# Optimization experiments

Hardware: AMD Instinct MI355X
Metric: run time of the kernel (lower is better)

## Reference

```python
import jax, jax.numpy as jnp
import numpy as np

B, H, F, G = 32768, 256, 32, 16
N = F * G * 2  # total number of heads


def setup_inputs() -> dict:
    key = jax.random.key(0)
    kx, kw, kb = jax.random.split(key, 3)
    x = jax.random.normal(kx, (B, H), dtype=jnp.float32)
    # stacked weights/biases of all N = in_features*granularity*2 Linear(H,1) heads
    W = jax.random.normal(kw, (N, H), dtype=jnp.float32) * (1.0 / jnp.sqrt(H))
    b = jax.random.normal(kb, (N,), dtype=jnp.float32) * 0.01
    return {"x": x, "W": W, "b": b}


def reference(x, W, b):
    # Fused equivalent of N independent Linear(H,1)+Sigmoid heads:
    # one [B,H] x [H,N] matmul + bias + sigmoid, then reshape to [B,F,G,2].
    z = jax.nn.sigmoid(jnp.einsum("bh,nh->bn", x, W) + b)
    return z.reshape(x.shape[0], F, G, 2)
```

## Files before the change

### kernel.cpp

```cpp
#include <hip/hip_runtime.h>
#include <hip/hip_fp16.h>

typedef _Float16 half8 __attribute__((ext_vector_type(8)));
typedef _Float16 half4 __attribute__((ext_vector_type(4)));
typedef float floatx4 __attribute__((ext_vector_type(4)));

#define KH 256
#define NN 1024
#define BM 64
#define BN 64
#define LDW 264
#define NT (NN / BN)

__global__ __launch_bounds__(256, 2)
void lfh_kernel(const float* __restrict__ x, const float* __restrict__ W,
                const float* __restrict__ bias, float* __restrict__ out) {
    __shared__ _Float16 Ws[2][BN * LDW];

    const int t   = threadIdx.x;
    const int w   = t >> 6;
    const int l   = t & 63;
    const int l15 = l & 15;
    const int lq  = l >> 4;
    const int m0  = blockIdx.x * BM;

    half8 afrag[8];
    {
        const int arow = m0 + w * 16 + l15;
        const float* xr = x + (size_t)arow * KH;
        #pragma unroll
        for (int ks = 0; ks < 8; ++ks) {
            const int kb = ks * 32 + lq * 8;
            floatx4 lo = *(const floatx4*)(xr + kb);
            floatx4 hi = *(const floatx4*)(xr + kb + 4);
            half8 f;
            f[0] = (_Float16)lo[0]; f[1] = (_Float16)lo[1];
            f[2] = (_Float16)lo[2]; f[3] = (_Float16)lo[3];
            f[4] = (_Float16)hi[0]; f[5] = (_Float16)hi[1];
            f[6] = (_Float16)hi[2]; f[7] = (_Float16)hi[3];
            afrag[ks] = f;
        }
    }

    #pragma unroll
    for (int j = 0; j < 16; ++j) {
        const int flat = j * 1024 + t * 4;
        const int nl = flat >> 8, k = flat & 255;
        floatx4 v = *(const floatx4*)(W + (size_t)nl * KH + k);
        half4 h;
        h[0] = (_Float16)v[0]; h[1] = (_Float16)v[1];
        h[2] = (_Float16)v[2]; h[3] = (_Float16)v[3];
        *(half4*)&Ws[0][nl * LDW + k] = h;
    }
    __syncthreads();

    int cur = 0;
    for (int nt = 0; nt < NT; ++nt) {
        const int n0 = nt * BN;

        floatx4 wreg[16];
        if (nt + 1 < NT) {
            const float* Wn = W + (size_t)(n0 + BN) * KH;
            #pragma unroll
            for (int j = 0; j < 16; ++j) {
                const int flat = j * 1024 + t * 4;
                wreg[j] = *(const floatx4*)(Wn + ((flat >> 8) * KH + (flat & 255)));
            }
        }

        floatx4 acc[4];
        #pragma unroll
        for (int nf = 0; nf < 4; ++nf) acc[nf] = (floatx4)0.0f;

        #pragma unroll
        for (int ks = 0; ks < 8; ++ks) {
            #pragma unroll
            for (int nf = 0; nf < 4; ++nf) {
                half8 wf = *(const half8*)&Ws[cur][(nf * 16 + l15) * LDW + ks * 32 + lq * 8];
                acc[nf] = __builtin_amdgcn_mfma_f32_16x16x32_f16(afrag[ks], wf, acc[nf], 0, 0, 0);
            }
        }

        if (nt + 1 < NT) {
            #pragma unroll
            for (int j = 0; j < 16; ++j) {
                const int flat = j * 1024 + t * 4;
                const int nl = flat >> 8, k = flat & 255;
                half4 h;
                h[0] = (_Float16)wreg[j][0]; h[1] = (_Float16)wreg[j][1];
                h[2] = (_Float16)wreg[j][2]; h[3] = (_Float16)wreg[j][3];
                *(half4*)&Ws[cur ^ 1][nl * LDW + k] = h;
            }
        }
        __syncthreads();

        #pragma unroll
        for (int nf = 0; nf < 4; ++nf) {
            const int col = n0 + nf * 16 + l15;
            const float bv = bias[col];
            #pragma unroll
            for (int j = 0; j < 4; ++j) {
                const int row = m0 + w * 16 + lq * 4 + j;
                const float z = acc[nf][j] + bv;
                out[(size_t)row * NN + col] = 1.0f / (1.0f + __expf(-z));
            }
        }
        cur ^= 1;
    }
}

extern "C" void kernel_launch(void* const* d_in, const int* in_sizes, int n_in,
                              void* d_out, int out_size, void* d_ws, size_t ws_size,
                              hipStream_t stream) {
    const float* x = (const float*)d_in[0];
    const float* W = (const float*)d_in[1];
    const float* b = (const float*)d_in[2];
    float* out = (float*)d_out;
    const int Btot = in_sizes[0] / KH;
    dim3 grid(Btot / BM), block(256);
    lfh_kernel<<<grid, block, 0, stream>>>(x, W, b, out);
}
```

Measured before the change: 54.24 us.

## Prepack W to fp16 fragment layout and stream it into LDS directly

```diff
diff --git a/kernel.cpp b/kernel.cpp
--- a/kernel.cpp
+++ b/kernel.cpp
@@ -2,20 +2,38 @@
 #include <hip/hip_fp16.h>
 
 typedef _Float16 half8 __attribute__((ext_vector_type(8)));
-typedef _Float16 half4 __attribute__((ext_vector_type(4)));
 typedef float floatx4 __attribute__((ext_vector_type(4)));
 
 #define KH 256
 #define NN 1024
 #define BM 64
-#define BN 64
-#define LDW 264
-#define NT (NN / BN)
+#define STN 64
+#define NST (NN / STN)
+#define ST_F16 (STN * KH)
+
+__global__ __launch_bounds__(256)
+void pack_w(const float* __restrict__ W, _Float16* __restrict__ P) {
+    const int u  = blockIdx.x * 256 + threadIdx.x;
+    const int g  = u >> 9;
+    const int ks = (u >> 6) & 7;
+    const int l  = u & 63;
+    const int n  = g * 16 + (l & 15);
+    const int kb = ks * 32 + ((l >> 4) << 3);
+    const float* src = W + (size_t)n * KH + kb;
+    floatx4 lo = *(const floatx4*)src;
+    floatx4 hi = *(const floatx4*)(src + 4);
+    half8 h;
+    h[0] = (_Float16)lo[0]; h[1] = (_Float16)lo[1];
+    h[2] = (_Float16)lo[2]; h[3] = (_Float16)lo[3];
+    h[4] = (_Float16)hi[0]; h[5] = (_Float16)hi[1];
+    h[6] = (_Float16)hi[2]; h[7] = (_Float16)hi[3];
+    *(half8*)(P + (size_t)u * 8) = h;
+}
 
 __global__ __launch_bounds__(256, 2)
-void lfh_kernel(const float* __restrict__ x, const float* __restrict__ W,
-                const float* __restrict__ bias, float* __restrict__ out) {
-    __shared__ _Float16 Ws[2][BN * LDW];
+void lfh_main(const float* __restrict__ x, const _Float16* __restrict__ P,
+              const float* __restrict__ bias, float* __restrict__ out) {
+    __shared__ _Float16 Ws[2][ST_F16];
 
     const int t   = threadIdx.x;
     const int w   = t >> 6;
@@ -23,11 +41,11 @@
     const int l15 = l & 15;
     const int lq  = l >> 4;
     const int m0  = blockIdx.x * BM;
+    const int brow = m0 + w * 16 + l15;
 
     half8 afrag[8];
     {
-        const int arow = m0 + w * 16 + l15;
-        const float* xr = x + (size_t)arow * KH;
+        const float* xr = x + (size_t)brow * KH;
         #pragma unroll
         for (int ks = 0; ks < 8; ++ks) {
             const int kb = ks * 32 + lq * 8;
@@ -42,69 +60,44 @@
         }
     }
 
-    #pragma unroll
-    for (int j = 0; j < 16; ++j) {
-        const int flat = j * 1024 + t * 4;
-        const int nl = flat >> 8, k = flat & 255;
-        floatx4 v = *(const floatx4*)(W + (size_t)nl * KH + k);
-        half4 h;
-        h[0] = (_Float16)v[0]; h[1] = (_Float16)v[1];
-        h[2] = (_Float16)v[2]; h[3] = (_Float16)v[3];
-        *(half4*)&Ws[0][nl * LDW + k] = h;
-    }
+    auto stage = [&](int st, _Float16* dst) {
+        const _Float16* gsrc = P + (size_t)st * ST_F16;
+        #pragma unroll
+        for (int r = 0; r < 8; ++r) {
+            __builtin_amdgcn_global_load_lds(
+                (const __attribute__((address_space(1))) void*)(gsrc + r * 2048 + t * 8),
+                (__attribute__((address_space(3))) void*)(dst + r * 2048 + t * 8),
+                16, 0, 0);
+        }
+    };
+
+    stage(0, Ws[0]);
     __syncthreads();
 
     int cur = 0;
-    for (int nt = 0; nt < NT; ++nt) {
-        const int n0 = nt * BN;
+    for (int st = 0; st < NST; ++st) {
+        if (st + 1 < NST) stage(st + 1, Ws[cur ^ 1]);
 
-        floatx4 wreg[16];
-        if (nt + 1 < NT) {
-            const float* Wn = W + (size_t)(n0 + BN) * KH;
+        const _Float16* Bt = Ws[cur];
+        #pragma unroll
+        for (int nf = 0; nf < 4; ++nf) {
+            floatx4 acc = (floatx4)0.0f;
             #pragma unroll
-            for (int j = 0; j < 16; ++j) {
-                const int flat = j * 1024 + t * 4;
-                wreg[j] = *(const floatx4*)(Wn + ((flat >> 8) * KH + (flat & 255)));
+            for (int ks = 0; ks < 8; ++ks) {
+                half8 wf = *(const half8*)(Bt + ((nf * 8 + ks) * 64 + l) * 8);
+                acc = __builtin_amdgcn_mfma_f32_16x16x32_f16(wf, afrag[ks], acc, 0, 0, 0);
             }
-        }
-
-        floatx4 acc[4];
-        #pragma unroll
-        for (int nf = 0; nf < 4; ++nf) acc[nf] = (floatx4)0.0f;
-
-        #pragma unroll
-        for (int ks = 0; ks < 8; ++ks) {
+            const int nb = st * STN + nf * 16 + lq * 4;
+            floatx4 bv = *(const floatx4*)(bias + nb);
+            floatx4 r;
             #pragma unroll
-            for (int nf = 0; nf < 4; ++nf) {
-                half8 wf = *(const half8*)&Ws[cur][(nf * 16 + l15) * LDW + ks * 32 + lq * 8];
-                acc[nf] = __builtin_amdgcn_mfma_f32_16x16x32_f16(afrag[ks], wf, acc[nf], 0, 0, 0);
+            for (int j = 0; j < 4; ++j) {
+                const float z = acc[j] + bv[j];
+                r[j] = __builtin_amdgcn_rcpf(1.0f + __expf(-z));
             }
-        }
-
-        if (nt + 1 < NT) {
-            #pragma unroll
-            for (int j = 0; j < 16; ++j) {
-                const int flat = j * 1024 + t * 4;
-                const int nl = flat >> 8, k = flat & 255;
-                half4 h;
-                h[0] = (_Float16)wreg[j][0]; h[1] = (_Float16)wreg[j][1];
-                h[2] = (_Float16)wreg[j][2]; h[3] = (_Float16)wreg[j][3];
-                *(half4*)&Ws[cur ^ 1][nl * LDW + k] = h;
-            }
+            __builtin_nontemporal_store(r, (floatx4*)(out + (size_t)brow * NN + nb));
         }
         __syncthreads();
-
-        #pragma unroll
-        for (int nf = 0; nf < 4; ++nf) {
-            const int col = n0 + nf * 16 + l15;
-            const float bv = bias[col];
-            #pragma unroll
-            for (int j = 0; j < 4; ++j) {
-                const int row = m0 + w * 16 + lq * 4 + j;
-                const float z = acc[nf][j] + bv;
-                out[(size_t)row * NN + col] = 1.0f / (1.0f + __expf(-z));
-            }
-        }
         cur ^= 1;
     }
 }
@@ -116,7 +109,10 @@
     const float* W = (const float*)d_in[1];
     const float* b = (const float*)d_in[2];
     float* out = (float*)d_out;
+    _Float16* P = (_Float16*)d_ws;
+
+    pack_w<<<dim3(128), dim3(256), 0, stream>>>(W, P);
+
     const int Btot = in_sizes[0] / KH;
-    dim3 grid(Btot / BM), block(256);
-    lfh_kernel<<<grid, block, 0, stream>>>(x, W, b, out);
+    lfh_main<<<dim3(Btot / BM), dim3(256), 0, stream>>>(x, P, b, out);
 }
```

New measurement: 51.75 us. 4.6% less time.
